# Optimization experiments

Measured on AMD Instinct MI355X. Metric: run time of the kernel, lower is better.

Reference implementation:

```python
import jax, jax.numpy as jnp
import numpy as np

B = 524288  # batch size (number of ODE state samples)
D = 32      # state dimension (in_dim == out_dim forced by x.mm(weight) shape)


def setup_inputs() -> dict:
    key = jax.random.key(0)
    k1, k2, k3 = jax.random.split(key, 3)
    x = jax.random.normal(k1, (B, D), dtype=jnp.float32)
    # LinearODELayer weight, init uniform(-0.1, 0.1); used as x @ W_lin directly.
    W_lin = jax.random.uniform(k2, (D, D), dtype=jnp.float32, minval=-0.1, maxval=0.1)
    # NonLinearODELayer weight [D, D, D], init uniform(-0.001, 0.001).
    W_nl = jax.random.uniform(k3, (D, D, D), dtype=jnp.float32, minval=-0.001, maxval=0.001)
    return {"x": x, "W_lin": W_lin, "W_nl": W_nl}


def reference(x, W_lin, W_nl):
    # LinearODELayer: x.mm(weight) -> [B, D]
    lin = x @ W_lin
    # NonLinearODELayer: the matmul -> matmul(x.t()) -> permute -> diagonal -> t()
    # chain is exactly the batched bilinear form out[b, o] = x[b] @ W_nl[o] @ x[b].
    nl = jnp.einsum("bi,oij,bj->bo", x, W_nl, x)
    return lin + nl
```

## Files before the change

kernel.cpp:

```cpp
#include <hip/hip_runtime.h>


typedef __attribute__((ext_vector_type(8))) __bf16 bf16x8;
typedef __attribute__((ext_vector_type(4))) float floatx4;
typedef __attribute__((ext_vector_type(2))) float floatx2;

#define NB     524288
#define NTILES (NB / 16)
#define GRID   1024
#define ITERS  (NTILES / GRID)
#define REDW   544
#define REDB   (4 * REDW)

__device__ __forceinline__ int XW(int r, int e) {
    return r * 32 + ((((e >> 2) ^ (r & 7)) << 2) | (e & 3));
}

__device__ __forceinline__ bf16x8 pack8(floatx4 a, floatx4 b) {
    bf16x8 f;
    #pragma unroll
    for (int j = 0; j < 4; ++j) { f[j] = (__bf16)a[j]; f[j + 4] = (__bf16)b[j]; }
    return f;
}

__global__ __launch_bounds__(256, 4)
void nnode_kernel(const float* __restrict__ x, const float* __restrict__ Wlin,
                  const float* __restrict__ Wnl, float* __restrict__ out) {
    __shared__ __align__(16) float xs[2][512];
    __shared__ __align__(16) float red[2][REDB];

    const int tid  = threadIdx.x;
    const int wave = tid >> 6;
    const int lane = tid & 63;
    const int q    = lane >> 4;
    const int col  = lane & 15;

    bf16x8 bW[5][2];
    #pragma unroll
    for (int kl = 0; kl < 5; ++kl) {
        const int t  = wave * 5 + kl;
        const int p  = t >> 1, h = t & 1;
        const int pa = (p < 4) ? 0 : ((p < 7) ? 1 : ((p < 9) ? 2 : 3));
        const int pb = p - ((p < 4) ? 0 : ((p < 7) ? 3 : ((p < 9) ? 5 : 6)));
        const int i1 = 8 * pa + 4 * h + q;
        #pragma unroll
        for (int tt = 0; tt < 2; ++tt) {
            const float* base = Wnl + (size_t)(col + 16 * tt) * 1024;
            floatx4 v0 = *(const floatx4*)(base + i1 * 32 + 8 * pb);
            floatx4 v1 = *(const floatx4*)(base + i1 * 32 + 8 * pb + 4);
            if (pa != pb) {
                #pragma unroll
                for (int j = 0; j < 4; ++j) {
                    v0[j] += base[(size_t)(8 * pb + j) * 32 + i1];
                    v1[j] += base[(size_t)(8 * pb + 4 + j) * 32 + i1];
                }
            }
            bW[kl][tt] = pack8(v0, v1);
        }
    }

    bf16x8 bl0, bl1;
    #pragma unroll
    for (int j = 0; j < 8; ++j) {
        bl0[j] = (__bf16)(0.25f * Wlin[(q * 8 + j) * 32 + col]);
        bl1[j] = (__bf16)(0.25f * Wlin[(q * 8 + j) * 32 + col + 16]);
    }

    const bool q1 = (q & 1) != 0;
    const bool q2 = (q & 2) != 0;

    const int srow  = tid >> 4;
    const int scol2 = (tid & 15) * 2;

    {
        floatx2 v = *(const floatx2*)(x + (size_t)blockIdx.x * 512 + tid * 2);
        *(floatx2*)&xs[0][XW(srow, scol2)] = v;
    }
    __syncthreads();

    int it = 0;
    for (int tile = blockIdx.x; tile < NTILES; tile += GRID, ++it) {
        const int b0  = tile << 4;
        const int cur = it & 1;

        floatx2 pre;
        if (it < ITERS - 1)
            pre = *(const floatx2*)(x + ((size_t)b0 + GRID * 16) * 32 + tid * 2);

        const float* xb = xs[cur];
        floatx4 X[8];
        #pragma unroll
        for (int j = 0; j < 8; ++j)
            X[j] = *(const floatx4*)&xb[XW(col, 4 * j)];

        floatx4 acc0 = {0.f, 0.f, 0.f, 0.f};
        floatx4 acc1 = {0.f, 0.f, 0.f, 0.f};

        #define SELQ(V) (q2 ? (q1 ? (V)[3] : (V)[2]) : (q1 ? (V)[1] : (V)[0]))

        {
            floatx4 la0 = q2 ? (q1 ? X[6] : X[4]) : (q1 ? X[2] : X[0]);
            floatx4 la1 = q2 ? (q1 ? X[7] : X[5]) : (q1 ? X[3] : X[1]);
            bf16x8 af = pack8(la0, la1);
            acc0 = __builtin_amdgcn_mfma_f32_16x16x32_bf16(af, bl0, acc0, 0, 0, 0);
            acc1 = __builtin_amdgcn_mfma_f32_16x16x32_bf16(af, bl1, acc1, 0, 0, 0);
        }

        #define STEP(A, B, H, KL) {                                             \
            const float sc = SELQ(X[2 * (A) + (H)]);                            \
            floatx4 p0 = sc * X[2 * (B)];                                       \
            floatx4 p1 = sc * X[2 * (B) + 1];                                   \
            bf16x8 af = pack8(p0, p1);                                          \
            acc0 = __builtin_amdgcn_mfma_f32_16x16x32_bf16(af, bW[KL][0], acc0, 0, 0, 0); \
            acc1 = __builtin_amdgcn_mfma_f32_16x16x32_bf16(af, bW[KL][1], acc1, 0, 0, 0); }

        if (wave == 0) {
            STEP(0,0,0,0) STEP(0,0,1,1) STEP(0,1,0,2) STEP(0,1,1,3) STEP(0,2,0,4)
        } else if (wave == 1) {
            STEP(0,2,1,0) STEP(0,3,0,1) STEP(0,3,1,2) STEP(1,1,0,3) STEP(1,1,1,4)
        } else if (wave == 2) {
            STEP(1,2,0,0) STEP(1,2,1,1) STEP(1,3,0,2) STEP(1,3,1,3) STEP(2,2,0,4)
        } else {
            STEP(2,2,1,0) STEP(2,3,0,1) STEP(2,3,1,2) STEP(3,3,0,3) STEP(3,3,1,4)
        }
        #undef STEP
        #undef SELQ

        float* rp = red[cur] + wave * REDW;
        #pragma unroll
        for (int r = 0; r < 4; ++r) {
            rp[(q * 4 + r) * 34 + col]      = acc0[r];
            rp[(q * 4 + r) * 34 + col + 16] = acc1[r];
        }
        if (it < ITERS - 1)
            *(floatx2*)&xs[cur ^ 1][XW(srow, scol2)] = pre;
        __syncthreads();

        const float* rb = red[cur];
        floatx2 sum = *(const floatx2*)(rb + srow * 34 + scol2);
        #pragma unroll
        for (int w = 1; w < 4; ++w) {
            floatx2 pp = *(const floatx2*)(rb + w * REDW + srow * 34 + scol2);
            sum.x += pp.x; sum.y += pp.y;
        }
        *(floatx2*)(out + (size_t)b0 * 32 + tid * 2) = sum;
    }
}

extern "C" void kernel_launch(void* const* d_in, const int* in_sizes, int n_in,
                              void* d_out, int out_size, void* d_ws, size_t ws_size,
                              hipStream_t stream) {
    const float* x    = (const float*)d_in[0];
    const float* Wlin = (const float*)d_in[1];
    const float* Wnl  = (const float*)d_in[2];
    float* out        = (float*)d_out;
    nnode_kernel<<<dim3(GRID), dim3(256), 0, stream>>>(x, Wlin, Wnl, out);
}
```

Measured before the change: 162.7 us.

## Process two 16-row tiles per block with wave pairs splitting bilinear terms

Each block now handles 32 rows per iteration, with two pairs of waves each owning a 16-row tile and splitting the 20 bilinear K-steps ten per wave. This halves cross-wave reduction traffic (two partials instead of four) and widens global loads and stores to 16 bytes. In exchange each wave holds twice as many bf16 weight fragments in registers, so occupancy is lowered to 3 blocks per SM with a 768-block grid and uneven per-block chunk counts.

```diff
diff --git a/kernel.cpp b/kernel.cpp
--- a/kernel.cpp
+++ b/kernel.cpp
@@ -6,13 +6,11 @@
 typedef __attribute__((ext_vector_type(2))) float floatx2;
 
 #define NB     524288
-#define NTILES (NB / 16)
-#define GRID   1024
-#define ITERS  (NTILES / GRID)
+#define NCHUNK (NB / 32)
+#define GRID   768
 #define REDW   544
-#define REDB   (4 * REDW)
 
-__device__ __forceinline__ int XW(int r, int e) {
+__device__ __forceinline__ int XW32(int r, int e) {
     return r * 32 + ((((e >> 2) ^ (r & 7)) << 2) | (e & 3));
 }
 
@@ -23,22 +21,24 @@
     return f;
 }
 
-__global__ __launch_bounds__(256, 4)
+__global__ __launch_bounds__(256, 3)
 void nnode_kernel(const float* __restrict__ x, const float* __restrict__ Wlin,
                   const float* __restrict__ Wnl, float* __restrict__ out) {
-    __shared__ __align__(16) float xs[2][512];
-    __shared__ __align__(16) float red[2][REDB];
+    __shared__ __align__(16) float xs[2][1024];
+    __shared__ __align__(16) float red[2][2][2][REDW];
 
     const int tid  = threadIdx.x;
     const int wave = tid >> 6;
     const int lane = tid & 63;
     const int q    = lane >> 4;
     const int col  = lane & 15;
+    const int tile = wave >> 1;
+    const int w01  = wave & 1;
 
-    bf16x8 bW[5][2];
+    bf16x8 bW[10][2];
     #pragma unroll
-    for (int kl = 0; kl < 5; ++kl) {
-        const int t  = wave * 5 + kl;
+    for (int kl = 0; kl < 10; ++kl) {
+        const int t  = w01 * 10 + kl;
         const int p  = t >> 1, h = t & 1;
         const int pa = (p < 4) ? 0 : ((p < 7) ? 1 : ((p < 9) ? 2 : 3));
         const int pb = p - ((p < 4) ? 0 : ((p < 7) ? 3 : ((p < 9) ? 5 : 6)));
@@ -62,36 +62,40 @@
     bf16x8 bl0, bl1;
     #pragma unroll
     for (int j = 0; j < 8; ++j) {
-        bl0[j] = (__bf16)(0.25f * Wlin[(q * 8 + j) * 32 + col]);
-        bl1[j] = (__bf16)(0.25f * Wlin[(q * 8 + j) * 32 + col + 16]);
+        bl0[j] = (__bf16)(0.5f * Wlin[(q * 8 + j) * 32 + col]);
+        bl1[j] = (__bf16)(0.5f * Wlin[(q * 8 + j) * 32 + col + 16]);
     }
 
     const bool q1 = (q & 1) != 0;
     const bool q2 = (q & 2) != 0;
 
-    const int srow  = tid >> 4;
-    const int scol2 = (tid & 15) * 2;
+    const int sword = (tid >> 3) * 32 + (((tid & 7) ^ ((tid >> 3) & 7)) << 2);
+    const int xrow  = tile * 16 + col;
+    const int rT  = tid >> 7;
+    const int rr  = (tid >> 3) & 15;
+    const int rc4 = (tid & 7) * 4;
+
+    const int n = 21 + ((blockIdx.x < (NCHUNK - 21 * GRID)) ? 1 : 0);
 
     {
-        floatx2 v = *(const floatx2*)(x + (size_t)blockIdx.x * 512 + tid * 2);
-        *(floatx2*)&xs[0][XW(srow, scol2)] = v;
+        floatx4 v = *(const floatx4*)(x + (size_t)blockIdx.x * 1024 + tid * 4);
+        *(floatx4*)&xs[0][sword] = v;
     }
     __syncthreads();
 
-    int it = 0;
-    for (int tile = blockIdx.x; tile < NTILES; tile += GRID, ++it) {
-        const int b0  = tile << 4;
-        const int cur = it & 1;
+    int chunk = blockIdx.x;
+    for (int k = 0; k < n; ++k, chunk += GRID) {
+        const int cur = k & 1;
 
-        floatx2 pre;
-        if (it < ITERS - 1)
-            pre = *(const floatx2*)(x + ((size_t)b0 + GRID * 16) * 32 + tid * 2);
+        floatx4 pre;
+        if (k < n - 1)
+            pre = *(const floatx4*)(x + (size_t)(chunk + GRID) * 1024 + tid * 4);
 
         const float* xb = xs[cur];
         floatx4 X[8];
         #pragma unroll
         for (int j = 0; j < 8; ++j)
-            X[j] = *(const floatx4*)&xb[XW(col, 4 * j)];
+            X[j] = *(const floatx4*)&xb[XW32(xrow, 4 * j)];
 
         floatx4 acc0 = {0.f, 0.f, 0.f, 0.f};
         floatx4 acc1 = {0.f, 0.f, 0.f, 0.f};
@@ -114,36 +118,38 @@
             acc0 = __builtin_amdgcn_mfma_f32_16x16x32_bf16(af, bW[KL][0], acc0, 0, 0, 0); \
             acc1 = __builtin_amdgcn_mfma_f32_16x16x32_bf16(af, bW[KL][1], acc1, 0, 0, 0); }
 
-        if (wave == 0) {
+        if (w01 == 0) {
             STEP(0,0,0,0) STEP(0,0,1,1) STEP(0,1,0,2) STEP(0,1,1,3) STEP(0,2,0,4)
-        } else if (wave == 1) {
-            STEP(0,2,1,0) STEP(0,3,0,1) STEP(0,3,1,2) STEP(1,1,0,3) STEP(1,1,1,4)
-        } else if (wave == 2) {
+            STEP(0,2,1,5) STEP(0,3,0,6) STEP(0,3,1,7) STEP(1,1,0,8) STEP(1,1,1,9)
+        } else {
             STEP(1,2,0,0) STEP(1,2,1,1) STEP(1,3,0,2) STEP(1,3,1,3) STEP(2,2,0,4)
-        } else {
-            STEP(2,2,1,0) STEP(2,3,0,1) STEP(2,3,1,2) STEP(3,3,0,3) STEP(3,3,1,4)
+            STEP(2,2,1,5) STEP(2,3,0,6) STEP(2,3,1,7) STEP(3,3,0,8) STEP(3,3,1,9)
         }
         #undef STEP
         #undef SELQ
 
-        float* rp = red[cur] + wave * REDW;
-        #pragma unroll
-        for (int r = 0; r < 4; ++r) {
-            rp[(q * 4 + r) * 34 + col]      = acc0[r];
-            rp[(q * 4 + r) * 34 + col + 16] = acc1[r];
+        {
+            float* rp = &red[cur][tile][w01][0];
+            #pragma unroll
+            for (int r2 = 0; r2 < 4; ++r2) {
+                rp[(q * 4 + r2) * 34 + col]      = acc0[r2];
+                rp[(q * 4 + r2) * 34 + col + 16] = acc1[r2];
+            }
         }
-        if (it < ITERS - 1)
-            *(floatx2*)&xs[cur ^ 1][XW(srow, scol2)] = pre;
+        if (k < n - 1)
+            *(floatx4*)&xs[cur ^ 1][sword] = pre;
         __syncthreads();
 
-        const float* rb = red[cur];
-        floatx2 sum = *(const floatx2*)(rb + srow * 34 + scol2);
-        #pragma unroll
-        for (int w = 1; w < 4; ++w) {
-            floatx2 pp = *(const floatx2*)(rb + w * REDW + srow * 34 + scol2);
-            sum.x += pp.x; sum.y += pp.y;
+        {
+            const float* b0p = &red[cur][rT][0][rr * 34 + rc4];
+            const float* b1p = &red[cur][rT][1][rr * 34 + rc4];
+            floatx2 u0 = *(const floatx2*)(b0p);
+            floatx2 u1 = *(const floatx2*)(b0p + 2);
+            floatx2 v0 = *(const floatx2*)(b1p);
+            floatx2 v1 = *(const floatx2*)(b1p + 2);
+            floatx4 s = {u0.x + v0.x, u0.y + v0.y, u1.x + v1.x, u1.y + v1.y};
+            *(floatx4*)(out + ((size_t)chunk * 32 + rT * 16 + rr) * 32 + rc4) = s;
         }
-        *(floatx2*)(out + (size_t)b0 * 32 + tid * 2) = sum;
     }
 }
 
```

Result: slower. 188.9 us (+16.0%).
